# Performance work log

Hardware: AMD Instinct MI355X
Metric: run time of the kernel (lower is better)

The kernel has to match this reference:

```python
import jax, jax.numpy as jnp
import numpy as np

HIDDEN_DIM = 768
N_HEAD = 12
ATTN_DIM = HIDDEN_DIM // N_HEAD  # 64
SCALE = jnp.sqrt(jnp.float32(ATTN_DIM))


def setup_inputs() -> dict:
    key = jax.random.key(0)
    ks = jax.random.split(key, 6)
    B, S = 8, 2048
    return {
        "query": jax.random.normal(ks[0], (B, S, HIDDEN_DIM), dtype=jnp.float32),
        "key": jax.random.normal(ks[1], (B, S, HIDDEN_DIM), dtype=jnp.float32),
        "value": jax.random.normal(ks[2], (B, S, HIDDEN_DIM), dtype=jnp.float32),
        "Wq": jax.random.normal(ks[3], (ATTN_DIM, HIDDEN_DIM), dtype=jnp.float32) * 0.02,
        "Wk": jax.random.normal(ks[4], (ATTN_DIM, HIDDEN_DIM), dtype=jnp.float32) * 0.02,
        "Wv": jax.random.normal(ks[5], (ATTN_DIM, HIDDEN_DIM), dtype=jnp.float32) * 0.02,
    }


def reference(query, key, value, Wq, Wk, Wv):
    # Linear projections (bias=False): x @ W.T -> [B, S, attn_dim]
    q = jnp.einsum("bsh,dh->bsd", query, Wq)
    k = jnp.einsum("bsh,dh->bsd", key, Wk)
    v = jnp.einsum("bsh,dh->bsd", value, Wv)
    # Scaled dot-product scores: [B, S, S]
    scores = jnp.einsum("bqd,bkd->bqk", q, k) / SCALE
    attn = jax.nn.softmax(scores, axis=-1)  # dropout p=0 -> identity in eval
    # Weighted sum of values: [B, S, attn_dim]
    return jnp.einsum("bqk,bkd->bqd", attn, v)
```

## Files before the change

### kernel.cpp

```cpp
#include <hip/hip_runtime.h>

typedef short s16x8 __attribute__((ext_vector_type(8)));
typedef float f32x4 __attribute__((ext_vector_type(4)));
typedef unsigned short us4 __attribute__((ext_vector_type(4)));

static __device__ __forceinline__ unsigned short f2bf(float f) {
  unsigned u = __builtin_bit_cast(unsigned, f);
  u += 0x7FFFu + ((u >> 16) & 1u);
  return (unsigned short)(u >> 16);
}

#if __has_builtin(__builtin_amdgcn_exp2f)
#define EXP2(x) __builtin_amdgcn_exp2f(x)
#else
#define EXP2(x) exp2f(x)
#endif

#define QSCALE 0.1803368801111204f

#define MFMA16(a, b, c) __builtin_amdgcn_mfma_f32_16x16x32_bf16((a), (b), (c), 0, 0, 0)

__global__ __launch_bounds__(256) void proj_kernel(
    const float* __restrict__ Xq, const float* __restrict__ Xk, const float* __restrict__ Xv,
    const float* __restrict__ Wq, const float* __restrict__ Wk, const float* __restrict__ Wv,
    unsigned short* __restrict__ qf,
    unsigned short* __restrict__ kf,
    unsigned short* __restrict__ vfo)
{
  __shared__ __align__(16) unsigned short xs[64][72];
  __shared__ __align__(16) unsigned short ws[64][72];

  const int bid = blockIdx.x;
  const int t = bid >> 8;
  const int rb = bid & 255;
  const int b = rb >> 5;
  const int stile = rb & 31;
  const float* X = (t == 0) ? Xq : (t == 1) ? Xk : Xv;
  const float* W = (t == 0) ? Wq : (t == 1) ? Wk : Wv;

  const int tid = threadIdx.x;
  const int wv = tid >> 6;
  const int lane = tid & 63;
  const int j = lane & 15;
  const int g = lane >> 4;

  f32x4 acc[4];
#pragma unroll
  for (int i = 0; i < 4; ++i) acc[i] = {0.f, 0.f, 0.f, 0.f};

  const size_t xrow0 = (size_t)b * 2048 + (size_t)stile * 64;

  for (int kc = 0; kc < 768; kc += 64) {
#pragma unroll
    for (int p = 0; p < 4; ++p) {
      int lin = p * 256 + tid;
      int row = lin >> 4;
      int seg = lin & 15;
      float4 xv = *(const float4*)(X + (xrow0 + row) * 768 + kc + seg * 4);
      us4 px; px.x = f2bf(xv.x); px.y = f2bf(xv.y); px.z = f2bf(xv.z); px.w = f2bf(xv.w);
      *(us4*)&xs[row][seg * 4] = px;
      float4 wv4 = *(const float4*)(W + (size_t)row * 768 + kc + seg * 4);
      us4 pw; pw.x = f2bf(wv4.x); pw.y = f2bf(wv4.y); pw.z = f2bf(wv4.z); pw.w = f2bf(wv4.w);
      *(us4*)&ws[row][seg * 4] = pw;
    }
    __syncthreads();
    s16x8 a0 = *(const s16x8*)&xs[wv * 16 + j][g * 8];
    s16x8 a1 = *(const s16x8*)&xs[wv * 16 + j][32 + g * 8];
#pragma unroll
    for (int ct = 0; ct < 4; ++ct) {
      s16x8 b0 = *(const s16x8*)&ws[ct * 16 + j][g * 8];
      s16x8 b1 = *(const s16x8*)&ws[ct * 16 + j][32 + g * 8];
      acc[ct] = MFMA16(a0, b0, acc[ct]);
      acc[ct] = MFMA16(a1, b1, acc[ct]);
    }
    __syncthreads();
  }

  unsigned short* fb = &xs[0][0];
  if (t < 2) {
    const float sc = (t == 0) ? QSCALE : 1.0f;
#pragma unroll
    for (int ct = 0; ct < 4; ++ct) {
      int base16 = wv * 1024 + ((ct >= 2) ? 512 : 0) + (((ct & 1) * 2 + (j >> 3)) * 128) + (j & 7);
#pragma unroll
      for (int r = 0; r < 4; ++r)
        fb[base16 + (g * 4 + r) * 8] = f2bf(acc[ct][r] * sc);
    }
    __syncthreads();
    unsigned short* dst = ((t == 0) ? qf : kf) + ((size_t)b * 128 + stile * 4) * 1024;
#pragma unroll
    for (int p2 = 0; p2 < 2; ++p2) {
      int idx = p2 * 2048 + tid * 8;
      *(s16x8*)(dst + idx) = *(const s16x8*)&fb[idx];
    }
  } else {
#pragma unroll
    for (int ct = 0; ct < 4; ++ct) {
      us4 pk;
      pk.x = f2bf(acc[ct][0]); pk.y = f2bf(acc[ct][1]);
      pk.z = f2bf(acc[ct][2]); pk.w = f2bf(acc[ct][3]);
      *(us4*)&fb[ct * 1024 + ((wv >= 2) ? 512 : 0) +
                 (((wv & 1) * 2 + (g >> 1)) * 16 + j) * 8 + (g & 1) * 4] = pk;
    }
    __syncthreads();
    unsigned short* gb = vfo + ((size_t)b * 32 + stile) * 4096;
#pragma unroll
    for (int p2 = 0; p2 < 2; ++p2) {
      int idx = p2 * 2048 + tid * 8;
      *(s16x8*)(gb + idx) = *(const s16x8*)&fb[idx];
    }
  }
}

__global__ __launch_bounds__(512, 4) void attn_kernel(
    const unsigned short* __restrict__ qf,
    const unsigned short* __restrict__ kf,
    const unsigned short* __restrict__ vf,
    float* __restrict__ out)
{
  __shared__ __align__(16) unsigned char raw[69632];
  __shared__ float lls[8][32];
  unsigned short* p_lds = (unsigned short*)raw;
  float* comb = (float*)raw;

  const int tid = threadIdx.x;
  const int wv = tid >> 6;
  const int lane = tid & 63;
  const int j = lane & 15;
  const int g = lane >> 4;
  const int sg = wv >> 2;
  const int c = wv & 3;

  const int bid0 = blockIdx.x;
  const int swz = (bid0 & 7) * 32 + (bid0 >> 3);
  const int b = swz >> 5;
  const int qt = swz & 31;

  s16x8 q0[2], q1[2];
#pragma unroll
  for (int rg = 0; rg < 2; ++rg) {
    const unsigned short* qp =
        qf + ((size_t)(b * 128 + qt * 4 + sg * 2 + rg)) * 1024 + lane * 8;
    q0[rg] = *(const s16x8*)(qp);
    q1[rg] = *(const s16x8*)(qp + 512);
  }

  f32x4 o[2][4];
#pragma unroll
  for (int rg = 0; rg < 2; ++rg)
#pragma unroll
    for (int i = 0; i < 4; ++i) o[rg][i] = {0.f, 0.f, 0.f, 0.f};
  float l_acc[2] = {0.f, 0.f};

  const unsigned short* kfb = kf + (size_t)b * 131072 + c * 32768 + lane * 8;
  const unsigned short* vfb = vf + (size_t)b * 131072 + c * 32768 + lane * 8;
  unsigned short* myp0 = p_lds + (size_t)((wv * 2 + 0) * 16 + j) * 72;
  unsigned short* myp1 = p_lds + (size_t)((wv * 2 + 1) * 16 + j) * 72;

  for (int kt = 0; kt < 8; ++kt) {
    const unsigned short* kc_ = kfb + kt * 4096;
    s16x8 ka[4], kb2[4];
#pragma unroll
    for (int ct = 0; ct < 4; ++ct) {
      ka[ct] = *(const s16x8*)(kc_ + ct * 1024);
      kb2[ct] = *(const s16x8*)(kc_ + ct * 1024 + 512);
    }
    {
      f32x4 st[4];
#pragma unroll
      for (int ct = 0; ct < 4; ++ct) {
        f32x4 z = {0.f, 0.f, 0.f, 0.f};
        z = MFMA16(ka[ct], q0[0], z);
        z = MFMA16(kb2[ct], q1[0], z);
        st[ct] = z;
      }
#pragma unroll
      for (int ct = 0; ct < 4; ++ct) {
        float p0 = EXP2(st[ct][0]);
        float p1 = EXP2(st[ct][1]);
        float p2 = EXP2(st[ct][2]);
        float p3 = EXP2(st[ct][3]);
        l_acc[0] += (p0 + p1) + (p2 + p3);
        us4 pk; pk.x = f2bf(p0); pk.y = f2bf(p1); pk.z = f2bf(p2); pk.w = f2bf(p3);
        *(us4*)&myp0[ct * 16 + g * 4] = pk;
      }
    }
    {
      f32x4 st[4];
#pragma unroll
      for (int ct = 0; ct < 4; ++ct) {
        f32x4 z = {0.f, 0.f, 0.f, 0.f};
        z = MFMA16(ka[ct], q0[1], z);
        z = MFMA16(kb2[ct], q1[1], z);
        st[ct] = z;
      }
#pragma unroll
      for (int ct = 0; ct < 4; ++ct) {
        float p0 = EXP2(st[ct][0]);
        float p1 = EXP2(st[ct][1]);
        float p2 = EXP2(st[ct][2]);
        float p3 = EXP2(st[ct][3]);
        l_acc[1] += (p0 + p1) + (p2 + p3);
        us4 pk; pk.x = f2bf(p0); pk.y = f2bf(p1); pk.z = f2bf(p2); pk.w = f2bf(p3);
        *(us4*)&myp1[ct * 16 + g * 4] = pk;
      }
    }
    const unsigned short* vc_ = vfb + kt * 4096;
    s16x8 va[4], vb2[4];
#pragma unroll
    for (int dt = 0; dt < 4; ++dt) {
      va[dt] = *(const s16x8*)(vc_ + dt * 1024);
      vb2[dt] = *(const s16x8*)(vc_ + dt * 1024 + 512);
    }
    s16x8 pa0 = *(const s16x8*)&myp0[g * 8];
    s16x8 pa1 = *(const s16x8*)&myp0[32 + g * 8];
#pragma unroll
    for (int dt = 0; dt < 4; ++dt) {
      o[0][dt] = MFMA16(pa0, va[dt], o[0][dt]);
      o[0][dt] = MFMA16(pa1, vb2[dt], o[0][dt]);
    }
    s16x8 pb0 = *(const s16x8*)&myp1[g * 8];
    s16x8 pb1 = *(const s16x8*)&myp1[32 + g * 8];
#pragma unroll
    for (int dt = 0; dt < 4; ++dt) {
      o[1][dt] = MFMA16(pb0, va[dt], o[1][dt]);
      o[1][dt] = MFMA16(pb1, vb2[dt], o[1][dt]);
    }
  }

#pragma unroll
  for (int rg = 0; rg < 2; ++rg) {
    l_acc[rg] += __shfl_xor(l_acc[rg], 16);
    l_acc[rg] += __shfl_xor(l_acc[rg], 32);
  }

  __syncthreads();
#pragma unroll
  for (int rg = 0; rg < 2; ++rg) {
#pragma unroll
    for (int dt = 0; dt < 4; ++dt)
#pragma unroll
      for (int r = 0; r < 4; ++r)
        comb[((size_t)wv * 32 + rg * 16 + g * 4 + r) * 68 + dt * 16 + j] = o[rg][dt][r];
    if (g == 0) lls[wv][rg * 16 + j] = l_acc[rg];
  }
  __syncthreads();

#pragma unroll
  for (int it = 0; it < 8; ++it) {
    const int idx = it * 512 + tid;
    const int row = idx >> 6;
    const int d = idx & 63;
    const int ssg = row >> 5;
    const int srow = row & 31;
    float s = 0.f, lt = 0.f;
#pragma unroll
    for (int cc = 0; cc < 4; ++cc) {
      s += comb[((size_t)(ssg * 4 + cc) * 32 + srow) * 68 + d];
      lt += lls[ssg * 4 + cc][srow];
    }
    out[(((size_t)b * 2048) + qt * 64 + row) * 64 + d] = s / lt;
  }
}

extern "C" void kernel_launch(void* const* d_in, const int* in_sizes, int n_in,
                              void* d_out, int out_size, void* d_ws, size_t ws_size,
                              hipStream_t stream) {
  const float* query = (const float*)d_in[0];
  const float* key_  = (const float*)d_in[1];
  const float* value = (const float*)d_in[2];
  const float* Wq = (const float*)d_in[3];
  const float* Wk = (const float*)d_in[4];
  const float* Wv = (const float*)d_in[5];

  unsigned short* qfb = (unsigned short*)d_ws;
  unsigned short* kfb = qfb + 1048576u;
  unsigned short* vfb = qfb + 2u * 1048576u;
  float* outp = (float*)d_out;

  hipLaunchKernelGGL(proj_kernel, dim3(768), dim3(256), 0, stream,
                     query, key_, value, Wq, Wk, Wv, qfb, kfb, vfb);
  hipLaunchKernelGGL(attn_kernel, dim3(256), dim3(512), 0, stream,
                     qfb, kfb, vfb, outp);
}
```

Before: 47.63 us.

## Use 4-wave attention blocks with each wave handling all 64 query rows

The attention kernel drops from 8 waves to 4 per block. Each wave now processes all four 16-row query groups against its quarter of the keys, so every K/V fragment loaded from global memory is reused across four query groups instead of two. The cross-wave combine is done in two halves to fit the smaller LDS buffer, and the output writes become vectorized float4 stores with a reciprocal multiply. The cost is more registers per wave (Q fragments and accumulators double) and fewer waves per block, which may reduce latency hiding with only 256 blocks.

```diff
diff --git a/kernel.cpp b/kernel.cpp
--- a/kernel.cpp
+++ b/kernel.cpp
@@ -112,14 +112,14 @@
   }
 }
 
-__global__ __launch_bounds__(512, 4) void attn_kernel(
+__global__ __launch_bounds__(256, 3) void attn_kernel(
     const unsigned short* __restrict__ qf,
     const unsigned short* __restrict__ kf,
     const unsigned short* __restrict__ vf,
     float* __restrict__ out)
 {
-  __shared__ __align__(16) unsigned char raw[69632];
-  __shared__ float lls[8][32];
+  __shared__ __align__(16) unsigned char raw[36864];
+  __shared__ float lls[4][32];
   unsigned short* p_lds = (unsigned short*)raw;
   float* comb = (float*)raw;
 
@@ -128,81 +128,53 @@
   const int lane = tid & 63;
   const int j = lane & 15;
   const int g = lane >> 4;
-  const int sg = wv >> 2;
-  const int c = wv & 3;
 
   const int bid0 = blockIdx.x;
   const int swz = (bid0 & 7) * 32 + (bid0 >> 3);
   const int b = swz >> 5;
   const int qt = swz & 31;
 
-  s16x8 q0[2], q1[2];
-#pragma unroll
-  for (int rg = 0; rg < 2; ++rg) {
+  s16x8 q0[4], q1[4];
+#pragma unroll
+  for (int rg = 0; rg < 4; ++rg) {
     const unsigned short* qp =
-        qf + ((size_t)(b * 128 + qt * 4 + sg * 2 + rg)) * 1024 + lane * 8;
+        qf + ((size_t)(b * 128 + qt * 4 + rg)) * 1024 + lane * 8;
     q0[rg] = *(const s16x8*)(qp);
     q1[rg] = *(const s16x8*)(qp + 512);
   }
 
-  f32x4 o[2][4];
-#pragma unroll
-  for (int rg = 0; rg < 2; ++rg)
+  f32x4 o[4][4];
+#pragma unroll
+  for (int rg = 0; rg < 4; ++rg)
 #pragma unroll
     for (int i = 0; i < 4; ++i) o[rg][i] = {0.f, 0.f, 0.f, 0.f};
-  float l_acc[2] = {0.f, 0.f};
-
-  const unsigned short* kfb = kf + (size_t)b * 131072 + c * 32768 + lane * 8;
-  const unsigned short* vfb = vf + (size_t)b * 131072 + c * 32768 + lane * 8;
-  unsigned short* myp0 = p_lds + (size_t)((wv * 2 + 0) * 16 + j) * 72;
-  unsigned short* myp1 = p_lds + (size_t)((wv * 2 + 1) * 16 + j) * 72;
+  float l_acc[4] = {0.f, 0.f, 0.f, 0.f};
+
+  const unsigned short* kfb = kf + (size_t)b * 131072 + wv * 32768 + lane * 8;
+  const unsigned short* vfb = vf + (size_t)b * 131072 + wv * 32768 + lane * 8;
+  unsigned short* myp[4];
+#pragma unroll
+  for (int rg = 0; rg < 4; ++rg)
+    myp[rg] = p_lds + (size_t)((wv * 4 + rg) * 16 + j) * 72;
 
   for (int kt = 0; kt < 8; ++kt) {
     const unsigned short* kc_ = kfb + kt * 4096;
-    s16x8 ka[4], kb2[4];
-#pragma unroll
-    for (int ct = 0; ct < 4; ++ct) {
-      ka[ct] = *(const s16x8*)(kc_ + ct * 1024);
-      kb2[ct] = *(const s16x8*)(kc_ + ct * 1024 + 512);
-    }
-    {
-      f32x4 st[4];
-#pragma unroll
-      for (int ct = 0; ct < 4; ++ct) {
+#pragma unroll
+    for (int ct = 0; ct < 4; ++ct) {
+      s16x8 ka = *(const s16x8*)(kc_ + ct * 1024);
+      s16x8 kb2 = *(const s16x8*)(kc_ + ct * 1024 + 512);
+#pragma unroll
+      for (int rg = 0; rg < 4; ++rg) {
         f32x4 z = {0.f, 0.f, 0.f, 0.f};
-        z = MFMA16(ka[ct], q0[0], z);
-        z = MFMA16(kb2[ct], q1[0], z);
-        st[ct] = z;
-      }
-#pragma unroll
-      for (int ct = 0; ct < 4; ++ct) {
-        float p0 = EXP2(st[ct][0]);
-        float p1 = EXP2(st[ct][1]);
-        float p2 = EXP2(st[ct][2]);
-        float p3 = EXP2(st[ct][3]);
-        l_acc[0] += (p0 + p1) + (p2 + p3);
+        z = MFMA16(ka, q0[rg], z);
+        z = MFMA16(kb2, q1[rg], z);
+        float p0 = EXP2(z[0]);
+        float p1 = EXP2(z[1]);
+        float p2 = EXP2(z[2]);
+        float p3 = EXP2(z[3]);
+        l_acc[rg] += (p0 + p1) + (p2 + p3);
         us4 pk; pk.x = f2bf(p0); pk.y = f2bf(p1); pk.z = f2bf(p2); pk.w = f2bf(p3);
-        *(us4*)&myp0[ct * 16 + g * 4] = pk;
-      }
-    }
-    {
-      f32x4 st[4];
-#pragma unroll
-      for (int ct = 0; ct < 4; ++ct) {
-        f32x4 z = {0.f, 0.f, 0.f, 0.f};
-        z = MFMA16(ka[ct], q0[1], z);
-        z = MFMA16(kb2[ct], q1[1], z);
-        st[ct] = z;
-      }
-#pragma unroll
-      for (int ct = 0; ct < 4; ++ct) {
-        float p0 = EXP2(st[ct][0]);
-        float p1 = EXP2(st[ct][1]);
-        float p2 = EXP2(st[ct][2]);
-        float p3 = EXP2(st[ct][3]);
-        l_acc[1] += (p0 + p1) + (p2 + p3);
-        us4 pk; pk.x = f2bf(p0); pk.y = f2bf(p1); pk.z = f2bf(p2); pk.w = f2bf(p3);
-        *(us4*)&myp1[ct * 16 + g * 4] = pk;
+        *(us4*)&myp[rg][ct * 16 + g * 4] = pk;
       }
     }
     const unsigned short* vc_ = vfb + kt * 4096;
@@ -212,54 +184,56 @@
       va[dt] = *(const s16x8*)(vc_ + dt * 1024);
       vb2[dt] = *(const s16x8*)(vc_ + dt * 1024 + 512);
     }
-    s16x8 pa0 = *(const s16x8*)&myp0[g * 8];
-    s16x8 pa1 = *(const s16x8*)&myp0[32 + g * 8];
-#pragma unroll
-    for (int dt = 0; dt < 4; ++dt) {
-      o[0][dt] = MFMA16(pa0, va[dt], o[0][dt]);
-      o[0][dt] = MFMA16(pa1, vb2[dt], o[0][dt]);
-    }
-    s16x8 pb0 = *(const s16x8*)&myp1[g * 8];
-    s16x8 pb1 = *(const s16x8*)&myp1[32 + g * 8];
-#pragma unroll
-    for (int dt = 0; dt < 4; ++dt) {
-      o[1][dt] = MFMA16(pb0, va[dt], o[1][dt]);
-      o[1][dt] = MFMA16(pb1, vb2[dt], o[1][dt]);
-    }
-  }
-
-#pragma unroll
-  for (int rg = 0; rg < 2; ++rg) {
+#pragma unroll
+    for (int rg = 0; rg < 4; ++rg) {
+      s16x8 pa0 = *(const s16x8*)&myp[rg][g * 8];
+      s16x8 pa1 = *(const s16x8*)&myp[rg][32 + g * 8];
+#pragma unroll
+      for (int dt = 0; dt < 4; ++dt) {
+        o[rg][dt] = MFMA16(pa0, va[dt], o[rg][dt]);
+        o[rg][dt] = MFMA16(pa1, vb2[dt], o[rg][dt]);
+      }
+    }
+  }
+
+#pragma unroll
+  for (int rg = 0; rg < 4; ++rg) {
     l_acc[rg] += __shfl_xor(l_acc[rg], 16);
     l_acc[rg] += __shfl_xor(l_acc[rg], 32);
   }
 
   __syncthreads();
-#pragma unroll
-  for (int rg = 0; rg < 2; ++rg) {
-#pragma unroll
-    for (int dt = 0; dt < 4; ++dt)
-#pragma unroll
-      for (int r = 0; r < 4; ++r)
-        comb[((size_t)wv * 32 + rg * 16 + g * 4 + r) * 68 + dt * 16 + j] = o[rg][dt][r];
-    if (g == 0) lls[wv][rg * 16 + j] = l_acc[rg];
-  }
-  __syncthreads();
-
-#pragma unroll
-  for (int it = 0; it < 8; ++it) {
-    const int idx = it * 512 + tid;
-    const int row = idx >> 6;
-    const int d = idx & 63;
-    const int ssg = row >> 5;
-    const int srow = row & 31;
-    float s = 0.f, lt = 0.f;
-#pragma unroll
-    for (int cc = 0; cc < 4; ++cc) {
-      s += comb[((size_t)(ssg * 4 + cc) * 32 + srow) * 68 + d];
-      lt += lls[ssg * 4 + cc][srow];
-    }
-    out[(((size_t)b * 2048) + qt * 64 + row) * 64 + d] = s / lt;
+
+#pragma unroll
+  for (int half = 0; half < 2; ++half) {
+#pragma unroll
+    for (int rg2 = 0; rg2 < 2; ++rg2) {
+      const int rg = half * 2 + rg2;
+#pragma unroll
+      for (int dt = 0; dt < 4; ++dt)
+#pragma unroll
+        for (int r = 0; r < 4; ++r)
+          comb[((size_t)wv * 32 + rg2 * 16 + g * 4 + r) * 68 + dt * 16 + j] = o[rg][dt][r];
+      if (g == 0) lls[wv][rg2 * 16 + j] = l_acc[rg];
+    }
+    __syncthreads();
+#pragma unroll
+    for (int it = 0; it < 2; ++it) {
+      const int idx = it * 1024 + tid * 4;
+      const int row = idx >> 6;
+      const int d0 = idx & 63;
+      f32x4 s = {0.f, 0.f, 0.f, 0.f};
+      float lt = 0.f;
+#pragma unroll
+      for (int cc = 0; cc < 4; ++cc) {
+        s += *(const f32x4*)&comb[((size_t)cc * 32 + row) * 68 + d0];
+        lt += lls[cc][row];
+      }
+      const float inv = 1.0f / lt;
+      f32x4 rr = s * inv;
+      *(f32x4*)&out[(((size_t)b * 2048) + qt * 64 + half * 32 + row) * 64 + d0] = rr;
+    }
+    __syncthreads();
   }
 }
 
@@ -280,6 +254,6 @@
 
   hipLaunchKernelGGL(proj_kernel, dim3(768), dim3(256), 0, stream,
                      query, key_, value, Wq, Wk, Wv, qfb, kfb, vfb);
-  hipLaunchKernelGGL(attn_kernel, dim3(256), dim3(512), 0, stream,
+  hipLaunchKernelGGL(attn_kernel, dim3(256), dim3(256), 0, stream,
                      qfb, kfb, vfb, outp);
 }
```

After: 58.30 us. 1.22x slower.
